# Kernel tuning notes

Measured on AMD Instinct MI355X. Metric: run time of the kernel, lower is better.

Reference implementation:

```python
import jax, jax.numpy as jnp
import numpy as np

C_TOTAL = 201      # n_classes + 1 (background)
N_CLASSES = 200
K = 5              # n_prototypes
DIM = 768
GAMMA = 0.999
TEMPERATURE = 0.2
THRESH = 0.8       # assignment_threshold


def l2norm(x, axis=-1, eps=1e-12):
    return x / jnp.maximum(jnp.linalg.norm(x, axis=axis, keepdims=True), eps)


def setup_inputs() -> dict:
    key = jax.random.key(0)
    k0, k1, k2, k3, k4 = jax.random.split(key, 5)
    B, H, W = 32, 32, 32
    N = H * W
    patch_tokens = jax.random.normal(k0, (B, N, DIM), jnp.float32)
    raw_patch_tokens = jax.random.normal(k1, (B, N, DIM), jnp.float32)
    # trunc_normal_(std=0.02) init of the prototype buffer
    prototypes = jax.random.truncated_normal(k2, -2.0, 2.0, (C_TOTAL, K, DIM), jnp.float32) * 0.02
    sa_weights = jnp.ones((N_CLASSES, K), jnp.float32)  # constant init -> uniform softmax, same as 0.5
    labels = jax.random.randint(k3, (32,), 0, N_CLASSES)
    sam_masks = jax.random.randint(k4, (B, H, W), 0, 2, dtype=jnp.int32)
    return {
        'patch_tokens': patch_tokens,
        'raw_patch_tokens': raw_patch_tokens,
        'prototypes': prototypes,
        'sa_weights': sa_weights,
        'labels': labels,
        'sam_masks': sam_masks,
    }


def reference(patch_tokens, raw_patch_tokens, prototypes, sa_weights, labels, sam_masks):
    B, N, D = patch_tokens.shape
    H = W = int(np.sqrt(N))

    # --- prototype matching ---
    pt = l2norm(patch_tokens)
    proto_n = l2norm(prototypes)
    # [B, N, C, K] cosine logits
    logits = jnp.einsum('bnd,ckd->bnck', pt, proto_n)
    image_prototype_logits = logits.max(axis=1)                    # [B, C, K]
    saw = jax.nn.softmax(sa_weights, axis=-1) * K                  # ScoreAggregation
    class_logits = (image_prototype_logits[:, :-1, :] * saw).sum(-1) / TEMPERATURE  # [B, n_classes]

    # --- pseudo patch labels (sam_masks already at (H, W) -> nearest interp is identity) ---
    pm = sam_masks.astype(jnp.float32)                             # [B, H, W]
    pseudo = jnp.where(pm == 1.0, labels[:, None, None], N_CLASSES)  # [B, H, W] int

    # --- online clustering (vectorized over the per-class python loop) ---
    raw = l2norm(raw_patch_tokens).reshape(B * N, D)               # detached in original
    lab_flat = pseudo.reshape(-1)                                  # [BN]
    L = logits.reshape(B * N, C_TOTAL, K)
    # gather each token's logits for its own (pseudo) class: L[n, lab_flat[n], :]
    Lc = jnp.take_along_axis(L, lab_flat[:, None, None], axis=1)[:, 0, :]  # [BN, K]
    A = jax.nn.softmax(Lc, axis=-1)
    max_vals = A.max(axis=-1)
    indices = A.argmax(axis=-1)
    # threshold then L1-renormalize (zero rows stay zero, matching F.normalize eps)
    A = jnp.where(max_vals[:, None] < THRESH, 0.0, A)
    A = A / jnp.maximum(A.sum(axis=-1, keepdims=True), 1e-12)
    # per-class soft-kmeans centroid accumulation: P_c_new = A_c^T @ I_c
    wx = A[:, :, None] * raw[:, None, :]                           # [BN, K, D]
    P_c_new = jax.ops.segment_sum(wx, lab_flat, num_segments=C_TOTAL)  # [C, K, D]
    counts = jax.ops.segment_sum(jnp.ones_like(lab_flat), lab_flat, num_segments=C_TOTAL)
    present = (counts > 0)[:, None, None]
    # momentum EMA update, only for classes present in the batch
    P_new = jnp.where(present, GAMMA * prototypes + (1.0 - GAMMA) * P_c_new, prototypes)

    part_assignment_maps = (indices + lab_flat * K).reshape(B, H * W)

    return (class_logits, image_prototype_logits, logits, part_assignment_maps, P_new, pseudo)
```

## Files before the change

kernel.cpp:

```cpp
#include <hip/hip_runtime.h>
#include <math.h>

#define Bv   32
#define Nv   1024
#define Dv   768
#define Cv   201
#define Kv   5
#define CKv  1005
#define BNv  32768
#define NCLS 200

#define OFF_CL     0
#define OFF_IPL    6400
#define OFF_LOG    38560
#define OFF_PART   32970400
#define OFF_PNEW   33003168
#define OFF_PSEUDO 33775008

typedef short bf16x8 __attribute__((ext_vector_type(8)));
typedef float f32x4  __attribute__((ext_vector_type(4)));
typedef float f32x4u __attribute__((ext_vector_type(4), aligned(4)));
typedef __attribute__((address_space(1))) const unsigned int g_u32;
typedef __attribute__((address_space(3))) unsigned int l_u32;

__device__ inline unsigned short f2bf(float f) {
  unsigned u = __float_as_uint(f);
  u += 0x7fffu + ((u >> 16) & 1u);
  return (unsigned short)(u >> 16);
}
__device__ inline unsigned fenc(float f) {
  unsigned u = __float_as_uint(f);
  return u ^ (((unsigned)((int)u >> 31)) | 0x80000000u);
}
__device__ inline float fdec(unsigned u) {
  unsigned bits = (u & 0x80000000u) ? (u ^ 0x80000000u) : ~u;
  return __uint_as_float(bits);
}

__global__ __launch_bounds__(256) void prep_kernel(
    const float* __restrict__ pt, const float* __restrict__ proto,
    unsigned short* __restrict__ Ah, unsigned short* __restrict__ Bh,
    int* __restrict__ zbuf, int zn, int ZB) {
  if ((int)blockIdx.x < ZB) {
    int i = blockIdx.x * 256 + threadIdx.x;
    if (i < zn) zbuf[i] = 0;
    return;
  }
  const int rbase = (blockIdx.x - ZB) * 16 + (threadIdx.x >> 6) * 4;
  const int l = threadIdx.x & 63;

  if (rbase < BNv) {
    const float* src = pt + (size_t)rbase * Dv;
    float4 v[4][3];
#pragma unroll
    for (int r = 0; r < 4; ++r)
#pragma unroll
      for (int i = 0; i < 3; ++i)
        v[r][i] = reinterpret_cast<const float4*>(src + (size_t)r * Dv)[i * 64 + l];
    float s[4];
#pragma unroll
    for (int r = 0; r < 4; ++r)
      s[r] = v[r][0].x * v[r][0].x + v[r][0].y * v[r][0].y + v[r][0].z * v[r][0].z + v[r][0].w * v[r][0].w
           + v[r][1].x * v[r][1].x + v[r][1].y * v[r][1].y + v[r][1].z * v[r][1].z + v[r][1].w * v[r][1].w
           + v[r][2].x * v[r][2].x + v[r][2].y * v[r][2].y + v[r][2].z * v[r][2].z + v[r][2].w * v[r][2].w;
#pragma unroll
    for (int off = 32; off > 0; off >>= 1)
#pragma unroll
      for (int r = 0; r < 4; ++r) s[r] += __shfl_xor(s[r], off);
#pragma unroll
    for (int r = 0; r < 4; ++r) {
      float inv = 1.0f / fmaxf(sqrtf(s[r]), 1e-12f);
      unsigned short* dst = Ah + (size_t)(rbase + r) * Dv;
#pragma unroll
      for (int i = 0; i < 3; ++i) {
        float a0 = v[r][i].x * inv, a1 = v[r][i].y * inv;
        float a2 = v[r][i].z * inv, a3 = v[r][i].w * inv;
        *reinterpret_cast<ushort4*>(dst + i * 256 + 4 * l) =
            make_ushort4(f2bf(a0), f2bf(a1), f2bf(a2), f2bf(a3));
      }
    }
    return;
  }
  if (rbase < BNv + 1024) {
    const int rp0 = rbase - BNv;
    float4 v[4][3];
#pragma unroll
    for (int r = 0; r < 4; ++r) {
      int rp = rp0 + r;
      int rs = (rp < CKv) ? rp : (CKv - 1);
      const float* src = proto + (size_t)rs * Dv;
#pragma unroll
      for (int i = 0; i < 3; ++i)
        v[r][i] = reinterpret_cast<const float4*>(src)[i * 64 + l];
    }
    float s[4];
#pragma unroll
    for (int r = 0; r < 4; ++r)
      s[r] = v[r][0].x * v[r][0].x + v[r][0].y * v[r][0].y + v[r][0].z * v[r][0].z + v[r][0].w * v[r][0].w
           + v[r][1].x * v[r][1].x + v[r][1].y * v[r][1].y + v[r][1].z * v[r][1].z + v[r][1].w * v[r][1].w
           + v[r][2].x * v[r][2].x + v[r][2].y * v[r][2].y + v[r][2].z * v[r][2].z + v[r][2].w * v[r][2].w;
#pragma unroll
    for (int off = 32; off > 0; off >>= 1)
#pragma unroll
      for (int r = 0; r < 4; ++r) s[r] += __shfl_xor(s[r], off);
#pragma unroll
    for (int r = 0; r < 4; ++r) {
      int rp = rp0 + r;
      unsigned short* dst = Bh + (size_t)rp * Dv;
      float inv = (rp < CKv) ? 1.0f / fmaxf(sqrtf(s[r]), 1e-12f) : 0.0f;
#pragma unroll
      for (int i = 0; i < 3; ++i) {
        float a0 = v[r][i].x * inv, a1 = v[r][i].y * inv;
        float a2 = v[r][i].z * inv, a3 = v[r][i].w * inv;
        ushort4 w = (rp < CKv)
            ? make_ushort4(f2bf(a0), f2bf(a1), f2bf(a2), f2bf(a3))
            : make_ushort4(0, 0, 0, 0);
        *reinterpret_cast<ushort4*>(dst + i * 256 + 4 * l) = w;
      }
    }
    return;
  }
}

#define BM 256
#define BN 128
__global__ __launch_bounds__(512) void gemm_mfma_kernel(
    const unsigned short* __restrict__ Ah, const unsigned short* __restrict__ Bh,
    const float* __restrict__ raw, float* __restrict__ inv_raw,
    float* __restrict__ Co, unsigned int* __restrict__ iplU) {
  __shared__ __align__(16) unsigned char smem[49152];
#define LA(b) ((unsigned short (*)[32])(smem + (b) * 16384))
#define LB(b) ((unsigned short (*)[32])(smem + 32768 + (b) * 8192))
  const int tid  = threadIdx.x;
  const int wid  = tid >> 6;
  const int lane = tid & 63;
  const int orig = blockIdx.x;

  if (orig >= 1024) {
    const int base_row = (orig - 1024) * 128 + wid * 16;
    for (int it = 0; it < 16; it += 2) {
      const float* s0p = raw + (size_t)(base_row + it) * Dv;
      const float* s1p = s0p + Dv;
      float4 v[2][3];
#pragma unroll
      for (int i = 0; i < 3; ++i)
        v[0][i] = reinterpret_cast<const float4*>(s0p)[i * 64 + lane];
#pragma unroll
      for (int i = 0; i < 3; ++i)
        v[1][i] = reinterpret_cast<const float4*>(s1p)[i * 64 + lane];
      float s[2];
#pragma unroll
      for (int r = 0; r < 2; ++r)
        s[r] = v[r][0].x * v[r][0].x + v[r][0].y * v[r][0].y + v[r][0].z * v[r][0].z + v[r][0].w * v[r][0].w
             + v[r][1].x * v[r][1].x + v[r][1].y * v[r][1].y + v[r][1].z * v[r][1].z + v[r][1].w * v[r][1].w
             + v[r][2].x * v[r][2].x + v[r][2].y * v[r][2].y + v[r][2].z * v[r][2].z + v[r][2].w * v[r][2].w;
#pragma unroll
      for (int off = 32; off > 0; off >>= 1) {
        s[0] += __shfl_xor(s[0], off);
        s[1] += __shfl_xor(s[1], off);
      }
      if (lane == 0) {
        inv_raw[base_row + it]     = 1.0f / fmaxf(sqrtf(s[0]), 1e-12f);
        inv_raw[base_row + it + 1] = 1.0f / fmaxf(sqrtf(s[1]), 1e-12f);
      }
    }
    return;
  }

  const int wm = wid >> 1, wn = wid & 1;
  const int wgid = ((orig & 7) << 7) | (orig >> 3);
  const int m0 = (wgid >> 3) * BM, n0 = (wgid & 7) * BN;
  const int fr = lane & 15;
  const int q  = lane >> 4;

  f32x4 acc[4][4];
#pragma unroll
  for (int i = 0; i < 4; ++i)
#pragma unroll
    for (int j = 0; j < 4; ++j)
#pragma unroll
      for (int r = 0; r < 4; ++r) acc[i][j][r] = 0.f;

  const int ra = wid * 16 + (lane >> 2);
  const int sa = (lane & 3) ^ ((ra >> 1) & 3);
  const unsigned short* srcA0 = Ah + (size_t)(m0 + ra) * Dv + sa * 8;
  const unsigned short* srcA1 = Ah + (size_t)(m0 + 128 + ra) * Dv + sa * 8;
  const unsigned short* srcB0 = Bh + (size_t)(n0 + ra) * Dv + sa * 8;

#define STG_A0(buf, t) __builtin_amdgcn_global_load_lds((g_u32*)(srcA0 + (t) * 32), \
    (l_u32*)&LA(buf)[wid * 16][0], 16, 0, 0)
#define STG_A1(buf, t) __builtin_amdgcn_global_load_lds((g_u32*)(srcA1 + (t) * 32), \
    (l_u32*)&LA(buf)[128 + wid * 16][0], 16, 0, 0)
#define STG_B0(buf, t) __builtin_amdgcn_global_load_lds((g_u32*)(srcB0 + (t) * 32), \
    (l_u32*)&LB(buf)[wid * 16][0], 16, 0, 0)

  const int slotR = (q ^ ((fr >> 1) & 3)) * 8;

  STG_A0(0, 0); STG_A1(0, 0); STG_B0(0, 0);

#pragma unroll 2
  for (int t = 0; t < 24; ++t) {
    const int cur = t & 1;
    if (t < 23) {
      STG_A0(cur ^ 1, t + 1); STG_A1(cur ^ 1, t + 1); STG_B0(cur ^ 1, t + 1);
      asm volatile("s_waitcnt vmcnt(3)" ::: "memory");
    } else {
      asm volatile("s_waitcnt vmcnt(0)" ::: "memory");
    }
    __builtin_amdgcn_s_barrier();
    __builtin_amdgcn_sched_barrier(0);

    bf16x8 a[4];
#pragma unroll
    for (int ph = 0; ph < 2; ++ph) {
      if (ph == 0) {
#pragma unroll
        for (int i = 0; i < 4; ++i)
          a[i] = *reinterpret_cast<const bf16x8*>(&LA(cur)[wm * 64 + i * 16 + fr][slotR]);
      }
      bf16x8 b0 = *reinterpret_cast<const bf16x8*>(&LB(cur)[wn * 64 + (ph * 2) * 16 + fr][slotR]);
      bf16x8 b1 = *reinterpret_cast<const bf16x8*>(&LB(cur)[wn * 64 + (ph * 2 + 1) * 16 + fr][slotR]);
      asm volatile("s_waitcnt lgkmcnt(0)" ::: "memory");
      __builtin_amdgcn_sched_barrier(0);
      __builtin_amdgcn_s_setprio(1);
#pragma unroll
      for (int i = 0; i < 4; ++i) {
        acc[i][ph * 2]     = __builtin_amdgcn_mfma_f32_16x16x32_bf16(a[i], b0, acc[i][ph * 2], 0, 0, 0);
        acc[i][ph * 2 + 1] = __builtin_amdgcn_mfma_f32_16x16x32_bf16(a[i], b1, acc[i][ph * 2 + 1], 0, 0, 0);
      }
      __builtin_amdgcn_s_setprio(0);
      __builtin_amdgcn_sched_barrier(0);
      __builtin_amdgcn_s_barrier();
      __builtin_amdgcn_sched_barrier(0);
    }
  }
#undef STG_A0
#undef STG_A1
#undef STG_B0

  const int b_img = m0 >> 10;
#pragma unroll
  for (int j = 0; j < 4; ++j) {
    int n = n0 + wn * 64 + j * 16 + fr;
    bool ok = (n < CKv);
    float cmax = -INFINITY;
#pragma unroll
    for (int i = 0; i < 4; ++i)
#pragma unroll
      for (int r = 0; r < 4; ++r) cmax = fmaxf(cmax, acc[i][j][r]);
    cmax = fmaxf(cmax, __shfl_xor(cmax, 16));
    cmax = fmaxf(cmax, __shfl_xor(cmax, 32));
    if (lane < 16 && ok)
      atomicMax(&iplU[(size_t)b_img * 1024 + n], fenc(cmax));
  }

  float (*ebuf)[132] = (float (*)[132])smem;
  const int r2 = lane >> 5;
  const int cl = (lane & 31) * 4;
#pragma unroll
  for (int p = 0; p < 4; ++p) {
    __syncthreads();
    if (wm == p) {
#pragma unroll
      for (int i = 0; i < 4; ++i)
#pragma unroll
        for (int j = 0; j < 4; ++j)
#pragma unroll
          for (int r = 0; r < 4; ++r)
            ebuf[i * 16 + q * 4 + r][wn * 64 + j * 16 + fr] = acc[i][j][r];
    }
    __syncthreads();
#pragma unroll
    for (int rr = 0; rr < 8; rr += 2) {
      int row = wid * 8 + rr + r2;
      f32x4 v = *reinterpret_cast<const f32x4*>(&ebuf[row][cl]);
      int gc = n0 + cl;
      size_t base = (size_t)(m0 + p * 64 + row) * CKv + gc;
      if (gc + 3 < CKv) {
        *reinterpret_cast<f32x4u*>(&Co[base]) = v;
      } else {
#pragma unroll
        for (int e = 0; e < 4; ++e)
          if (gc + e < CKv) Co[base + e] = v[e];
      }
    }
  }
#undef LA
#undef LB
}

__global__ __launch_bounds__(256) void accum_fused_kernel(
    const float* __restrict__ logits, const int* __restrict__ labels,
    const int* __restrict__ sam, const float* __restrict__ raw,
    const float* __restrict__ inv_raw, float* __restrict__ out,
    float* __restrict__ P_acc, int* __restrict__ present,
    const unsigned int* __restrict__ iplU, const float* __restrict__ sa_w) {
  const int b = blockIdx.x;
  const int y = blockIdx.y;
  const int z = blockIdx.z;
  if (z == 8) {
    if (y != 0) return;
    int c = threadIdx.x;
    if (c >= Cv) return;
    float r[Kv];
#pragma unroll
    for (int k = 0; k < Kv; ++k) {
      r[k] = fdec(iplU[(size_t)b * 1024 + c * Kv + k]);
      out[OFF_IPL + (size_t)(b * Cv + c) * Kv + k] = r[k];
    }
    if (c < NCLS) {
      float w[Kv], wm = -INFINITY;
#pragma unroll
      for (int k = 0; k < Kv; ++k) { w[k] = sa_w[c * Kv + k]; wm = fmaxf(wm, w[k]); }
      float es = 0.f;
#pragma unroll
      for (int k = 0; k < Kv; ++k) { w[k] = expf(w[k] - wm); es += w[k]; }
      float cl = 0.f;
#pragma unroll
      for (int k = 0; k < Kv; ++k) cl += r[k] * (w[k] / es * (float)Kv);
      out[OFF_CL + b * NCLS + c] = cl / 0.2f;
    }
    return;
  }

  __shared__ float As[128][Kv];
  __shared__ float Sc[128];
  __shared__ int   Ls[128];
  const int t0 = z * 128;
  if (threadIdx.x < 128) {
    int n = b * Nv + t0 + threadIdx.x;
    int lab = (sam[n] == 1) ? labels[b] : NCLS;
    const float* p = logits + (size_t)n * CKv + lab * Kv;
    float L[Kv];
#pragma unroll
    for (int k = 0; k < Kv; ++k) L[k] = p[k];
    float mv = L[0];
    int idx = 0;
#pragma unroll
    for (int k = 1; k < Kv; ++k)
      if (L[k] > mv) { mv = L[k]; idx = k; }
    float e[Kv], s = 0.f;
#pragma unroll
    for (int k = 0; k < Kv; ++k) { e[k] = expf(L[k] - mv); s += e[k]; }
    float inv = 1.0f / s;
    float scale = (inv < 0.8f) ? 0.f : inv;
#pragma unroll
    for (int k = 0; k < Kv; ++k) As[threadIdx.x][k] = e[k] * scale;
    Ls[threadIdx.x] = lab;
    Sc[threadIdx.x] = inv_raw[n];
    if (y == 0) {
      out[OFF_PSEUDO + n] = (float)lab;
      out[OFF_PART + n] = (float)(idx + lab * Kv);
      present[lab] = 1;
    }
  }
  __syncthreads();

  const int d = y * 256 + threadIdx.x;
  float accL[Kv] = {}, accB[Kv] = {};
#pragma unroll 4
  for (int t = 0; t < 128; ++t) {
    int n2 = b * Nv + t0 + t;
    float rv = raw[(size_t)n2 * Dv + d] * Sc[t];
    if (Ls[t] == NCLS) {
#pragma unroll
      for (int k = 0; k < Kv; ++k) accB[k] = fmaf(As[t][k], rv, accB[k]);
    } else {
#pragma unroll
      for (int k = 0; k < Kv; ++k) accL[k] = fmaf(As[t][k], rv, accL[k]);
    }
  }
  int lab = labels[b];
#pragma unroll
  for (int k = 0; k < Kv; ++k) atomicAdd(&P_acc[((size_t)lab * Kv + k) * Dv + d], accL[k]);
#pragma unroll
  for (int k = 0; k < Kv; ++k) atomicAdd(&P_acc[((size_t)NCLS * Kv + k) * Dv + d], accB[k]);
}

__global__ __launch_bounds__(256) void pnew_kernel(
    const float* __restrict__ proto, const float* __restrict__ P_acc,
    const int* __restrict__ present, float* __restrict__ out) {
  int i = blockIdx.x * 256 + threadIdx.x;
  if (i >= Cv * Kv * Dv) return;
  int c = i / (Kv * Dv);
  float p = proto[i];
  out[OFF_PNEW + i] = present[c] ? 0.999f * p + 0.001f * P_acc[i] : p;
}

extern "C" void kernel_launch(void* const* d_in, const int* in_sizes, int n_in,
                              void* d_out, int out_size, void* d_ws, size_t ws_size,
                              hipStream_t stream) {
  const float* pt     = (const float*)d_in[0];
  const float* raw    = (const float*)d_in[1];
  const float* proto  = (const float*)d_in[2];
  const float* sa_w   = (const float*)d_in[3];
  const int*   labels = (const int*)d_in[4];
  const int*   sam    = (const int*)d_in[5];
  float* out = (float*)d_out;

  float* A_buf   = (float*)d_ws;
  int*   tok_lab = (int*)(A_buf + (size_t)BNv * Kv);
  float* P_acc   = (float*)(tok_lab + BNv);
  int*   present = (int*)(P_acc + (size_t)Cv * Kv * Dv);
  unsigned int* iplU = (unsigned int*)(present + 256);
  float* inv_raw = (float*)(iplU + BNv);
  unsigned short* Ah = (unsigned short*)(inv_raw + BNv);
  unsigned short* Bh = Ah + (size_t)BNv * Dv;

  int nz = Cv * Kv * Dv + 256 + BNv;
  int ZB = (nz + 255) / 256;
  int prep_rows_blocks = (BNv + 1024) / 16;

  prep_kernel<<<ZB + prep_rows_blocks, 256, 0, stream>>>(
      pt, proto, Ah, Bh, (int*)P_acc, nz, ZB);

  gemm_mfma_kernel<<<1024 + 256, 512, 0, stream>>>(
      Ah, Bh, raw, inv_raw, out + OFF_LOG, iplU);

  accum_fused_kernel<<<dim3(Bv, Dv / 256, 9), 256, 0, stream>>>(
      out + OFF_LOG, labels, sam, raw, inv_raw, out, P_acc, present, iplU, sa_w);

  pnew_kernel<<<(Cv * Kv * Dv + 255) / 256, 256, 0, stream>>>(
      proto, P_acc, present, out);
}
```

Measured before the change: 176.2 us.

## Fuse patch-token normalization and bf16 conversion into the GEMM A-tile load

Removes the prep pass that normalized patch tokens into a bf16 staging buffer. The GEMM now reads fp32 patch tokens directly, converts them to bf16 in registers, writes them to LDS, and accumulates the sum of squares. The per-row inverse norm is applied to the accumulators in the epilogue. This drops one full read and write of the 32768x768 activations. In exchange, the A tile is single-buffered with register prefetch and a full vmcnt(0) wait each K step, which reduces load/compute overlap. Scaling after the bf16 product instead of before also changes rounding slightly.

```diff
diff --git a/kernel.cpp b/kernel.cpp
--- a/kernel.cpp
+++ b/kernel.cpp
@@ -38,99 +38,60 @@
 }
 
 __global__ __launch_bounds__(256) void prep_kernel(
-    const float* __restrict__ pt, const float* __restrict__ proto,
-    unsigned short* __restrict__ Ah, unsigned short* __restrict__ Bh,
+    const float* __restrict__ proto, unsigned short* __restrict__ Bh,
     int* __restrict__ zbuf, int zn, int ZB) {
   if ((int)blockIdx.x < ZB) {
     int i = blockIdx.x * 256 + threadIdx.x;
     if (i < zn) zbuf[i] = 0;
     return;
   }
-  const int rbase = (blockIdx.x - ZB) * 16 + (threadIdx.x >> 6) * 4;
+  const int rp0 = (blockIdx.x - ZB) * 16 + (threadIdx.x >> 6) * 4;
   const int l = threadIdx.x & 63;
-
-  if (rbase < BNv) {
-    const float* src = pt + (size_t)rbase * Dv;
-    float4 v[4][3];
-#pragma unroll
-    for (int r = 0; r < 4; ++r)
-#pragma unroll
-      for (int i = 0; i < 3; ++i)
-        v[r][i] = reinterpret_cast<const float4*>(src + (size_t)r * Dv)[i * 64 + l];
-    float s[4];
-#pragma unroll
-    for (int r = 0; r < 4; ++r)
-      s[r] = v[r][0].x * v[r][0].x + v[r][0].y * v[r][0].y + v[r][0].z * v[r][0].z + v[r][0].w * v[r][0].w
-           + v[r][1].x * v[r][1].x + v[r][1].y * v[r][1].y + v[r][1].z * v[r][1].z + v[r][1].w * v[r][1].w
-           + v[r][2].x * v[r][2].x + v[r][2].y * v[r][2].y + v[r][2].z * v[r][2].z + v[r][2].w * v[r][2].w;
-#pragma unroll
-    for (int off = 32; off > 0; off >>= 1)
-#pragma unroll
-      for (int r = 0; r < 4; ++r) s[r] += __shfl_xor(s[r], off);
-#pragma unroll
-    for (int r = 0; r < 4; ++r) {
-      float inv = 1.0f / fmaxf(sqrtf(s[r]), 1e-12f);
-      unsigned short* dst = Ah + (size_t)(rbase + r) * Dv;
-#pragma unroll
-      for (int i = 0; i < 3; ++i) {
-        float a0 = v[r][i].x * inv, a1 = v[r][i].y * inv;
-        float a2 = v[r][i].z * inv, a3 = v[r][i].w * inv;
-        *reinterpret_cast<ushort4*>(dst + i * 256 + 4 * l) =
-            make_ushort4(f2bf(a0), f2bf(a1), f2bf(a2), f2bf(a3));
-      }
-    }
-    return;
-  }
-  if (rbase < BNv + 1024) {
-    const int rp0 = rbase - BNv;
-    float4 v[4][3];
-#pragma unroll
-    for (int r = 0; r < 4; ++r) {
-      int rp = rp0 + r;
-      int rs = (rp < CKv) ? rp : (CKv - 1);
-      const float* src = proto + (size_t)rs * Dv;
-#pragma unroll
-      for (int i = 0; i < 3; ++i)
-        v[r][i] = reinterpret_cast<const float4*>(src)[i * 64 + l];
-    }
-    float s[4];
-#pragma unroll
-    for (int r = 0; r < 4; ++r)
-      s[r] = v[r][0].x * v[r][0].x + v[r][0].y * v[r][0].y + v[r][0].z * v[r][0].z + v[r][0].w * v[r][0].w
-           + v[r][1].x * v[r][1].x + v[r][1].y * v[r][1].y + v[r][1].z * v[r][1].z + v[r][1].w * v[r][1].w
-           + v[r][2].x * v[r][2].x + v[r][2].y * v[r][2].y + v[r][2].z * v[r][2].z + v[r][2].w * v[r][2].w;
-#pragma unroll
-    for (int off = 32; off > 0; off >>= 1)
-#pragma unroll
-      for (int r = 0; r < 4; ++r) s[r] += __shfl_xor(s[r], off);
-#pragma unroll
-    for (int r = 0; r < 4; ++r) {
-      int rp = rp0 + r;
-      unsigned short* dst = Bh + (size_t)rp * Dv;
-      float inv = (rp < CKv) ? 1.0f / fmaxf(sqrtf(s[r]), 1e-12f) : 0.0f;
-#pragma unroll
-      for (int i = 0; i < 3; ++i) {
-        float a0 = v[r][i].x * inv, a1 = v[r][i].y * inv;
-        float a2 = v[r][i].z * inv, a3 = v[r][i].w * inv;
-        ushort4 w = (rp < CKv)
-            ? make_ushort4(f2bf(a0), f2bf(a1), f2bf(a2), f2bf(a3))
-            : make_ushort4(0, 0, 0, 0);
-        *reinterpret_cast<ushort4*>(dst + i * 256 + 4 * l) = w;
-      }
-    }
-    return;
+  if (rp0 >= 1024) return;
+  float4 v[4][3];
+#pragma unroll
+  for (int r = 0; r < 4; ++r) {
+    int rp = rp0 + r;
+    int rs = (rp < CKv) ? rp : (CKv - 1);
+    const float* src = proto + (size_t)rs * Dv;
+#pragma unroll
+    for (int i = 0; i < 3; ++i)
+      v[r][i] = reinterpret_cast<const float4*>(src)[i * 64 + l];
+  }
+  float s[4];
+#pragma unroll
+  for (int r = 0; r < 4; ++r)
+    s[r] = v[r][0].x * v[r][0].x + v[r][0].y * v[r][0].y + v[r][0].z * v[r][0].z + v[r][0].w * v[r][0].w
+         + v[r][1].x * v[r][1].x + v[r][1].y * v[r][1].y + v[r][1].z * v[r][1].z + v[r][1].w * v[r][1].w
+         + v[r][2].x * v[r][2].x + v[r][2].y * v[r][2].y + v[r][2].z * v[r][2].z + v[r][2].w * v[r][2].w;
+#pragma unroll
+  for (int off = 32; off > 0; off >>= 1)
+#pragma unroll
+    for (int r = 0; r < 4; ++r) s[r] += __shfl_xor(s[r], off);
+#pragma unroll
+  for (int r = 0; r < 4; ++r) {
+    int rp = rp0 + r;
+    unsigned short* dst = Bh + (size_t)rp * Dv;
+    float inv = (rp < CKv) ? 1.0f / fmaxf(sqrtf(s[r]), 1e-12f) : 0.0f;
+#pragma unroll
+    for (int i = 0; i < 3; ++i) {
+      float a0 = v[r][i].x * inv, a1 = v[r][i].y * inv;
+      float a2 = v[r][i].z * inv, a3 = v[r][i].w * inv;
+      ushort4 w = (rp < CKv)
+          ? make_ushort4(f2bf(a0), f2bf(a1), f2bf(a2), f2bf(a3))
+          : make_ushort4(0, 0, 0, 0);
+      *reinterpret_cast<ushort4*>(dst + i * 256 + 4 * l) = w;
+    }
   }
 }
 
 #define BM 256
 #define BN 128
 __global__ __launch_bounds__(512) void gemm_mfma_kernel(
-    const unsigned short* __restrict__ Ah, const unsigned short* __restrict__ Bh,
+    const float* __restrict__ pt, const unsigned short* __restrict__ Bh,
     const float* __restrict__ raw, float* __restrict__ inv_raw,
     float* __restrict__ Co, unsigned int* __restrict__ iplU) {
   __shared__ __align__(16) unsigned char smem[49152];
-#define LA(b) ((unsigned short (*)[32])(smem + (b) * 16384))
-#define LB(b) ((unsigned short (*)[32])(smem + 32768 + (b) * 8192))
   const int tid  = threadIdx.x;
   const int wid  = tid >> 6;
   const int lane = tid & 63;
@@ -167,6 +128,8 @@
     return;
   }
 
+  unsigned short (*lA)[32] = (unsigned short (*)[32])smem;
+#define LB(b) ((unsigned short (*)[32])(smem + 16384 + (b) * 8192))
   const int wm = wid >> 1, wn = wid & 1;
   const int wgid = ((orig & 7) << 7) | (orig >> 3);
   const int m0 = (wgid >> 3) * BM, n0 = (wgid & 7) * BN;
@@ -181,42 +144,68 @@
 #pragma unroll
       for (int r = 0; r < 4; ++r) acc[i][j][r] = 0.f;
 
+  const int r_own = tid >> 1;
+  const int h_own = tid & 1;
+  const float* srcAf = pt + (size_t)(m0 + r_own) * Dv + h_own * 16;
+  const int sl0 = (h_own * 2)     ^ ((r_own >> 1) & 3);
+  const int sl1 = (h_own * 2 + 1) ^ ((r_own >> 1) & 3);
+  unsigned short* wp0 = &lA[r_own][sl0 * 8];
+  unsigned short* wp1 = &lA[r_own][sl1 * 8];
+
   const int ra = wid * 16 + (lane >> 2);
   const int sa = (lane & 3) ^ ((ra >> 1) & 3);
-  const unsigned short* srcA0 = Ah + (size_t)(m0 + ra) * Dv + sa * 8;
-  const unsigned short* srcA1 = Ah + (size_t)(m0 + 128 + ra) * Dv + sa * 8;
   const unsigned short* srcB0 = Bh + (size_t)(n0 + ra) * Dv + sa * 8;
-
-#define STG_A0(buf, t) __builtin_amdgcn_global_load_lds((g_u32*)(srcA0 + (t) * 32), \
-    (l_u32*)&LA(buf)[wid * 16][0], 16, 0, 0)
-#define STG_A1(buf, t) __builtin_amdgcn_global_load_lds((g_u32*)(srcA1 + (t) * 32), \
-    (l_u32*)&LA(buf)[128 + wid * 16][0], 16, 0, 0)
 #define STG_B0(buf, t) __builtin_amdgcn_global_load_lds((g_u32*)(srcB0 + (t) * 32), \
     (l_u32*)&LB(buf)[wid * 16][0], 16, 0, 0)
 
   const int slotR = (q ^ ((fr >> 1) & 3)) * 8;
 
-  STG_A0(0, 0); STG_A1(0, 0); STG_B0(0, 0);
-
-#pragma unroll 2
+  float ssq = 0.f;
+  float4 af0, af1, af2, af3;
+#define LOAD_A(t) do {                                                   \
+    const float* ap_ = srcAf + (t) * 32;                                 \
+    af0 = *reinterpret_cast<const float4*>(ap_);                         \
+    af1 = *reinterpret_cast<const float4*>(ap_ + 4);                     \
+    af2 = *reinterpret_cast<const float4*>(ap_ + 8);                     \
+    af3 = *reinterpret_cast<const float4*>(ap_ + 12);                    \
+  } while (0)
+
+  LOAD_A(0);
+  STG_B0(0, 0);
+
   for (int t = 0; t < 24; ++t) {
     const int cur = t & 1;
-    if (t < 23) {
-      STG_A0(cur ^ 1, t + 1); STG_A1(cur ^ 1, t + 1); STG_B0(cur ^ 1, t + 1);
-      asm volatile("s_waitcnt vmcnt(3)" ::: "memory");
-    } else {
-      asm volatile("s_waitcnt vmcnt(0)" ::: "memory");
-    }
+    asm volatile("s_waitcnt vmcnt(0)" ::: "memory");
+    {
+      unsigned short t0[8], t1[8];
+      float x;
+#pragma unroll
+      for (int e = 0; e < 4; ++e) {
+        x = ((const float*)&af0)[e]; ssq = fmaf(x, x, ssq); t0[e]     = f2bf(x);
+        x = ((const float*)&af1)[e]; ssq = fmaf(x, x, ssq); t0[4 + e] = f2bf(x);
+        x = ((const float*)&af2)[e]; ssq = fmaf(x, x, ssq); t1[e]     = f2bf(x);
+        x = ((const float*)&af3)[e]; ssq = fmaf(x, x, ssq); t1[4 + e] = f2bf(x);
+      }
+      *reinterpret_cast<bf16x8*>(wp0) = *reinterpret_cast<const bf16x8*>(t0);
+      *reinterpret_cast<bf16x8*>(wp1) = *reinterpret_cast<const bf16x8*>(t1);
+    }
+    asm volatile("s_waitcnt lgkmcnt(0)" ::: "memory");
+    __builtin_amdgcn_sched_barrier(0);
     __builtin_amdgcn_s_barrier();
     __builtin_amdgcn_sched_barrier(0);
 
+    if (t < 23) {
+      LOAD_A(t + 1);
+      STG_B0(cur ^ 1, t + 1);
+    }
+
     bf16x8 a[4];
 #pragma unroll
     for (int ph = 0; ph < 2; ++ph) {
       if (ph == 0) {
 #pragma unroll
         for (int i = 0; i < 4; ++i)
-          a[i] = *reinterpret_cast<const bf16x8*>(&LA(cur)[wm * 64 + i * 16 + fr][slotR]);
+          a[i] = *reinterpret_cast<const bf16x8*>(&lA[wm * 64 + i * 16 + fr][slotR]);
       }
       bf16x8 b0 = *reinterpret_cast<const bf16x8*>(&LB(cur)[wn * 64 + (ph * 2) * 16 + fr][slotR]);
       bf16x8 b1 = *reinterpret_cast<const bf16x8*>(&LB(cur)[wn * 64 + (ph * 2 + 1) * 16 + fr][slotR]);
@@ -233,10 +222,30 @@
       __builtin_amdgcn_s_barrier();
       __builtin_amdgcn_sched_barrier(0);
     }
-  }
-#undef STG_A0
-#undef STG_A1
+    asm volatile("s_waitcnt lgkmcnt(0)" ::: "memory");
+    __builtin_amdgcn_sched_barrier(0);
+  }
 #undef STG_B0
+#undef LOAD_A
+
+  float* inv_s = (float*)(smem + 34048);
+  {
+    float tot = ssq + __shfl_xor(ssq, 1);
+    if (h_own == 0) inv_s[r_own] = 1.0f / fmaxf(sqrtf(tot), 1e-12f);
+  }
+  __syncthreads();
+  float ia[4][4];
+#pragma unroll
+  for (int i = 0; i < 4; ++i)
+#pragma unroll
+    for (int r = 0; r < 4; ++r)
+      ia[i][r] = inv_s[wm * 64 + i * 16 + q * 4 + r];
+#pragma unroll
+  for (int i = 0; i < 4; ++i)
+#pragma unroll
+    for (int j = 0; j < 4; ++j)
+#pragma unroll
+      for (int r = 0; r < 4; ++r) acc[i][j][r] *= ia[i][r];
 
   const int b_img = m0 >> 10;
 #pragma unroll
@@ -285,7 +294,6 @@
       }
     }
   }
-#undef LA
 #undef LB
 }
 
@@ -404,18 +412,16 @@
   int*   present = (int*)(P_acc + (size_t)Cv * Kv * Dv);
   unsigned int* iplU = (unsigned int*)(present + 256);
   float* inv_raw = (float*)(iplU + BNv);
-  unsigned short* Ah = (unsigned short*)(inv_raw + BNv);
-  unsigned short* Bh = Ah + (size_t)BNv * Dv;
+  unsigned short* Bh = (unsigned short*)(inv_raw + BNv);
 
   int nz = Cv * Kv * Dv + 256 + BNv;
   int ZB = (nz + 255) / 256;
-  int prep_rows_blocks = (BNv + 1024) / 16;
-
-  prep_kernel<<<ZB + prep_rows_blocks, 256, 0, stream>>>(
-      pt, proto, Ah, Bh, (int*)P_acc, nz, ZB);
+
+  prep_kernel<<<ZB + 1024 / 16, 256, 0, stream>>>(
+      proto, Bh, (int*)P_acc, nz, ZB);
 
   gemm_mfma_kernel<<<1024 + 256, 512, 0, stream>>>(
-      Ah, Bh, raw, inv_raw, out + OFF_LOG, iplU);
+      pt, Bh, raw, inv_raw, out + OFF_LOG, iplU);
 
   accum_fused_kernel<<<dim3(Bv, Dv / 256, 9), 256, 0, stream>>>(
       out + OFF_LOG, labels, sam, raw, inv_raw, out, P_acc, present, iplU, sa_w);
```

Result: slower. 195.1 us (+10.7%).
